# Kernel optimization log

Hardware: AMD Instinct MI355X
Metric: run time of the kernel (lower is better)

## Reference

```python
import jax, jax.numpy as jnp
import numpy as np

N, E, H, EF, NG = 50000, 600000, 128, 4, 20
R_MIN, R_MAX = 0.0, 10.0

def setup_inputs() -> dict:
    key = jax.random.key(0)
    ks = jax.random.split(key, 20)
    s = lambda fi, fo: 1.0 / np.sqrt(fi)
    inp = {
        'h': jax.random.normal(ks[0], (N, H), jnp.float32),
        'x': jax.random.normal(ks[1], (N, 3), jnp.float32),
        'edge_index': jax.random.randint(ks[2], (2, E), 0, N, jnp.int32),
        'mask_ligand': jnp.ones((N,), jnp.float32),
        'edge_attr': jax.random.normal(ks[3], (E, EF), jnp.float32),
        # edge_mlp: Linear(2H+EF+NG,H) silu Linear(H,H) silu
        'We1': jax.random.normal(ks[4], (2*H+EF+NG, H), jnp.float32) * s(2*H+EF+NG, H),
        'be1': jnp.zeros((H,), jnp.float32),
        'We2': jax.random.normal(ks[5], (H, H), jnp.float32) * s(H, H),
        'be2': jnp.zeros((H,), jnp.float32),
        # edge_inf: Linear(H,1) sigmoid
        'Winf': jax.random.normal(ks[6], (H, 1), jnp.float32) * s(H, 1),
        'binf': jnp.zeros((1,), jnp.float32),
        # x_mlp: Linear(H,H) silu Linear(H,1,no bias, gain 0.001) tanh
        'Wx1': jax.random.normal(ks[7], (H, H), jnp.float32) * s(H, H),
        'bx1': jnp.zeros((H,), jnp.float32),
        'Wx2': jax.random.normal(ks[8], (H, 1), jnp.float32) * (0.001 * s(H, 1)),
        # node_mlp: Linear(2H,H) silu Linear(H,H)
        'Wn1': jax.random.normal(ks[9], (2*H, H), jnp.float32) * s(2*H, H),
        'bn1': jnp.zeros((H,), jnp.float32),
        'Wn2': jax.random.normal(ks[10], (H, H), jnp.float32) * s(H, H),
        'bn2': jnp.zeros((H,), jnp.float32),
    }
    return inp

def _gaussian_smearing(d):
    # d: [E,1] -> [E,NG]
    offset = jnp.linspace(R_MIN, R_MAX, NG, dtype=d.dtype)
    coeff = -0.5 / (offset[1] - offset[0]) ** 2
    return jnp.exp(coeff * (d - offset) ** 2)

def reference(h, x, edge_index, mask_ligand, edge_attr,
              We1, be1, We2, be2, Winf, binf, Wx1, bx1, Wx2,
              Wn1, bn1, Wn2, bn2):
    src, dst = edge_index[0], edge_index[1]
    hi, hj = h[dst], h[src]                      # [E,H]
    rel_x = x[dst] - x[src]                      # [E,3]
    d_sq = jnp.sum(rel_x ** 2, -1, keepdims=True)  # [E,1]
    d = jnp.sqrt(d_sq + 1e-8)
    d_feat = _gaussian_smearing(d)               # [E,NG]
    edge_feat = jnp.concatenate([d_feat, edge_attr], -1)
    inp = jnp.concatenate([hi, hj, edge_feat], -1)  # [E,2H+NG+EF]
    mij = jax.nn.silu(jax.nn.silu(inp @ We1 + be1) @ We2 + be2)  # [E,H]
    eij = jax.nn.sigmoid(mij @ Winf + binf)       # [E,1]
    n = h.shape[0]
    mi = jax.ops.segment_sum(mij * eij, dst, num_segments=n)  # [N,H]
    h_new = h + (jax.nn.silu(jnp.concatenate([mi, h], -1) @ Wn1 + bn1) @ Wn2 + bn2)
    gate = jnp.tanh(jax.nn.silu(mij @ Wx1 + bx1) @ Wx2)        # [E,1]
    delta_x = jax.ops.segment_sum(rel_x / (d + 1.0) * gate, dst, num_segments=n)
    x_new = x + delta_x * mask_ligand[:, None]
    return h_new, x_new
```

## Files before the change

### kernel.cpp

```cpp
#include <hip/hip_runtime.h>
#include <hip/hip_bf16.h>
#include <cstdint>

#define NN 50000
#define NE 600000
#define HD 128
#define NG 20
#define EF 4
#define K1 280
#define TILES (NE/64)
#define EGRID 512
#define ROWU 148
#define NTILE 782
#define SW(r) ((r) ^ (((r)>>3)&7))

typedef __attribute__((ext_vector_type(4))) float f32x4;
typedef __attribute__((ext_vector_type(8))) __bf16 bf16x8;
typedef __attribute__((ext_vector_type(4))) unsigned int u32x4;

__device__ __forceinline__ float fast_rcp(float x){ return __builtin_amdgcn_rcpf(x); }
__device__ __forceinline__ float silu_f(float x){ return x * fast_rcp(1.0f + __expf(-x)); }
__device__ __forceinline__ float sigmoid_f(float x){ return fast_rcp(1.0f + __expf(-x)); }
__device__ __forceinline__ float tanh_f(float x){ return 1.0f - 2.0f*fast_rcp(__expf(2.0f*x)+1.0f); }

__device__ __forceinline__ uint32_t pk2(float a, float b){
  uint32_t ua = __float_as_uint(a); ua += 0x7FFFu + ((ua>>16)&1u);
  uint32_t ub = __float_as_uint(b); ub += 0x7FFFu + ((ub>>16)&1u);
  return (ua>>16) | (ub & 0xFFFF0000u);
}
__device__ __forceinline__ uint16_t bfb(float a){
  uint32_t ua = __float_as_uint(a); ua += 0x7FFFu + ((ua>>16)&1u);
  return (uint16_t)(ua>>16);
}
__device__ __forceinline__ float bf2f(uint16_t b){ return __uint_as_float(((uint32_t)b)<<16); }
__device__ __forceinline__ f32x4 MF(u32x4 a, u32x4 b, f32x4 c){
  return __builtin_amdgcn_mfma_f32_16x16x32_bf16(
      __builtin_bit_cast(bf16x8, a), __builtin_bit_cast(bf16x8, b), c, 0, 0, 0);
}

#define EDGE_LDS_U32 (64*ROWU + 4096 + 4096 + 448)
#define EDGE_LDS_B (EDGE_LDS_U32*4)

__global__ void __launch_bounds__(256) h2bf_kernel(
    const float* __restrict__ h, uint32_t* __restrict__ hb)
{
  const size_t i = ((size_t)blockIdx.x*256 + threadIdx.x)*8;
  const float4 a = *reinterpret_cast<const float4*>(h + i);
  const float4 b = *reinterpret_cast<const float4*>(h + i + 4);
  u32x4 v = {pk2(a.x,a.y), pk2(a.z,a.w), pk2(b.x,b.y), pk2(b.z,b.w)};
  *reinterpret_cast<u32x4*>(hb + i/2) = v;
}

template<int BF16H>
__global__ void __launch_bounds__(512, 4) edge_kernel(
    const float* __restrict__ h, const uint32_t* __restrict__ hb,
    const float* __restrict__ x,
    const int* __restrict__ ei, const float* __restrict__ eattr,
    const float* __restrict__ We1, const float* __restrict__ be1,
    const float* __restrict__ We2, const float* __restrict__ be2,
    const float* __restrict__ Winf, const float* __restrict__ binf,
    const float* __restrict__ Wx1, const float* __restrict__ bx1,
    const float* __restrict__ Wx2, float* __restrict__ out)
{
  extern __shared__ uint32_t smem[];
  uint32_t* s_inp = smem;
  uint16_t* t1f   = (uint16_t*)(smem + 64*ROWU);
  uint16_t* mf_   = (uint16_t*)(smem + 64*ROWU + 4096);
  uint32_t* tl    = smem + 64*ROWU + 8192;
  int*   s_dst  = (int*)tl;
  float* s_rel  = (float*)(tl+64);
  float* s_dist = (float*)(tl+256);
  float* s_pe   = (float*)(tl+320);
  float* s_pg   = (float*)(tl+384);

  const int tid = threadIdx.x;
  const int w = tid >> 6, l = tid & 63;
  const int lo = l & 15, hi = l >> 4;
  const int col = w*16 + lo;
  const int r8 = tid >> 3, p8 = tid & 7;
  const int ks2 = w >> 1;
  const int lp  = ((w&1)*2 + (lo>>3))*16 + 4*hi;
  const int jj  = lo & 7;
  const int lsw = SW(l);

  u32x4 B1[9], B2[4], B3[4];
  #pragma unroll
  for (int ks = 0; ks < 9; ++ks){
    float f[8];
    #pragma unroll
    for (int j = 0; j < 8; ++j){
      const int k = ks*32 + hi*8 + j;
      f[j] = (k < K1) ? We1[k*HD + col] : 0.0f;
    }
    B1[ks] = {pk2(f[0],f[1]), pk2(f[2],f[3]), pk2(f[4],f[5]), pk2(f[6],f[7])};
  }
  #pragma unroll
  for (int ks = 0; ks < 4; ++ks){
    float f2[8], f3[8];
    #pragma unroll
    for (int j = 0; j < 8; ++j){
      const int k = ks*32 + hi*8 + j;
      f2[j] = We2[k*HD + col];
      f3[j] = Wx1[k*HD + col];
    }
    B2[ks] = {pk2(f2[0],f2[1]), pk2(f2[2],f2[3]), pk2(f2[4],f2[5]), pk2(f2[6],f2[7])};
    B3[ks] = {pk2(f3[0],f3[1]), pk2(f3[2],f3[3]), pk2(f3[4],f3[5]), pk2(f3[6],f3[7])};
  }
  const float vbe1 = be1[col], vbe2 = be2[col], vbx1 = bx1[col];
  const float wi = Winf[col], wx = Wx2[col], vbinf = binf[0];
  const float SP = 10.0f/19.0f;
  const float CO = -0.5f/(SP*SP);

  int pnode, psj = 0, pdj = 0;
  {
    const int ebase = blockIdx.x*64;
    pnode = (p8 < 4) ? ei[NE + ebase + r8] : ei[ebase + r8];
    if (tid < 64){ psj = ei[ebase + tid]; pdj = ei[NE + ebase + tid]; }
  }

  for (int t = blockIdx.x; t < TILES; t += EGRID){
    const int ebase = t*64;
    __syncthreads();

    if (tid < 64){
      const float ax = x[pdj*3+0]-x[psj*3+0];
      const float ay = x[pdj*3+1]-x[psj*3+1];
      const float az = x[pdj*3+2]-x[psj*3+2];
      const float dd = sqrtf(ax*ax + ay*ay + az*az + 1e-8f);
      s_dst[tid] = pdj;
      s_rel[3*tid+0]=ax; s_rel[3*tid+1]=ay; s_rel[3*tid+2]=az;
      s_dist[tid]=dd; s_pe[tid]=0.0f; s_pg[tid]=0.0f;
      float g[24];
      #pragma unroll
      for (int j = 0; j < 20; ++j){ const float a = dd - j*SP; g[j] = __expf(CO*a*a); }
      const float4 e4 = *reinterpret_cast<const float4*>(eattr + (size_t)(ebase+tid)*EF);
      g[20]=e4.x; g[21]=e4.y; g[22]=e4.z; g[23]=e4.w;
      uint32_t* gp = s_inp + tid*ROWU + 128;
      u32x4 g0v = {pk2(g[0],g[1]),  pk2(g[2],g[3]),  pk2(g[4],g[5]),  pk2(g[6],g[7])};
      u32x4 g1v = {pk2(g[8],g[9]),  pk2(g[10],g[11]),pk2(g[12],g[13]),pk2(g[14],g[15])};
      u32x4 g2v = {pk2(g[16],g[17]),pk2(g[18],g[19]),pk2(g[20],g[21]),pk2(g[22],g[23])};
      u32x4 g3v = {0,0,0,0};
      *reinterpret_cast<u32x4*>(gp)    = g0v;
      *reinterpret_cast<u32x4*>(gp+4)  = g1v;
      *reinterpret_cast<u32x4*>(gp+8)  = g2v;
      *reinterpret_cast<u32x4*>(gp+12) = g3v;
    }
    if (BF16H){
      const uint32_t* hw = hb + (size_t)pnode*(HD/2) + (p8&3)*16;
      uint32_t* dp = s_inp + r8*ROWU + p8*16;
      #pragma unroll
      for (int q = 0; q < 4; ++q)
        *reinterpret_cast<u32x4*>(dp + 4*q) = *reinterpret_cast<const u32x4*>(hw + 4*q);
    } else {
      const float* hp = h + (size_t)pnode*HD + (p8&3)*32;
      uint32_t* dp = s_inp + r8*ROWU + p8*16;
      #pragma unroll
      for (int q = 0; q < 4; ++q){
        const float4 va = *reinterpret_cast<const float4*>(hp + 8*q);
        const float4 vb = *reinterpret_cast<const float4*>(hp + 8*q + 4);
        u32x4 v = { pk2(va.x,va.y), pk2(va.z,va.w), pk2(vb.x,vb.y), pk2(vb.z,vb.w) };
        *reinterpret_cast<u32x4*>(dp + 4*q) = v;
      }
    }
    int np = pnode, ns = psj, nd = pdj;
    if (t + EGRID < TILES){
      const int nb = (t + EGRID)*64;
      np = (p8 < 4) ? ei[NE + nb + r8] : ei[nb + r8];
      if (tid < 64){ ns = ei[nb + tid]; nd = ei[NE + nb + tid]; }
    }
    __syncthreads();

    #pragma unroll
    for (int Mt = 0; Mt < 4; ++Mt){
      const uint32_t* arow = s_inp + (Mt*16 + lo)*ROWU + hi*4;
      f32x4 acc = {0,0,0,0};
      #pragma unroll
      for (int ks = 0; ks < 9; ++ks)
        acc = MF(*reinterpret_cast<const u32x4*>(arow + ks*16), B1[ks], acc);
      #pragma unroll
      for (int reg = 0; reg < 4; ++reg)
        t1f[((Mt*4 + ks2)*64 + SW(lp+reg))*8 + jj] = bfb(silu_f(acc[reg] + vbe1));
    }
    __syncthreads();

    #pragma unroll
    for (int Mt = 0; Mt < 4; ++Mt){
      f32x4 acc = {0,0,0,0};
      #pragma unroll
      for (int ks = 0; ks < 4; ++ks)
        acc = MF(*reinterpret_cast<const u32x4*>(t1f + ((Mt*4+ks)*64 + lsw)*8), B2[ks], acc);
      float p[4];
      #pragma unroll
      for (int reg = 0; reg < 4; ++reg){
        const float m = silu_f(acc[reg] + vbe2);
        mf_[((Mt*4 + ks2)*64 + SW(lp+reg))*8 + jj] = bfb(m);
        p[reg] = m * wi;
      }
      #pragma unroll
      for (int msk = 1; msk < 16; msk <<= 1){
        #pragma unroll
        for (int reg = 0; reg < 4; ++reg) p[reg] += __shfl_xor(p[reg], msk);
      }
      if (lo == 0){
        #pragma unroll
        for (int reg = 0; reg < 4; ++reg) atomicAdd(&s_pe[Mt*16 + 4*hi + reg], p[reg]);
      }
    }
    __syncthreads();

    #pragma unroll
    for (int Mt = 0; Mt < 4; ++Mt){
      #pragma unroll
      for (int reg = 0; reg < 4; ++reg){
        const int r = Mt*16 + 4*hi + reg;
        const float eij = sigmoid_f(s_pe[r] + vbinf);
        const float m = bf2f(mf_[((Mt*4 + ks2)*64 + SW(lp+reg))*8 + jj]);
        atomicAdd(out + (size_t)s_dst[r]*HD + col, m*eij);
      }
    }
    #pragma unroll
    for (int Mt = 0; Mt < 4; ++Mt){
      f32x4 acc = {0,0,0,0};
      #pragma unroll
      for (int ks = 0; ks < 4; ++ks)
        acc = MF(*reinterpret_cast<const u32x4*>(mf_ + ((Mt*4+ks)*64 + lsw)*8), B3[ks], acc);
      float p[4];
      #pragma unroll
      for (int reg = 0; reg < 4; ++reg)
        p[reg] = silu_f(acc[reg] + vbx1) * wx;
      #pragma unroll
      for (int msk = 1; msk < 16; msk <<= 1){
        #pragma unroll
        for (int reg = 0; reg < 4; ++reg) p[reg] += __shfl_xor(p[reg], msk);
      }
      if (lo == 0){
        #pragma unroll
        for (int reg = 0; reg < 4; ++reg) atomicAdd(&s_pg[Mt*16 + 4*hi + reg], p[reg]);
      }
    }
    __syncthreads();

    if (tid < 192){
      const int er = tid/3, c = tid - 3*er;
      const float gate = tanh_f(s_pg[er]);
      const float sc = gate * fast_rcp(s_dist[er] + 1.0f);
      atomicAdd(out + (size_t)NN*HD + (size_t)s_dst[er]*3 + c, s_rel[3*er+c]*sc);
    }

    pnode = np; psj = ns; pdj = nd;
  }
}

#define CROW 132

__global__ void __launch_bounds__(512, 4) node_kernel(
    const float* __restrict__ h, const float* __restrict__ x,
    const float* __restrict__ mask,
    const float* __restrict__ Wn1, const float* __restrict__ bn1,
    const float* __restrict__ Wn2, const float* __restrict__ bn2,
    float* __restrict__ out)
{
  __shared__ uint32_t s_cat[64*CROW];
  __shared__ __align__(16) uint16_t t1n[4*4*64*8];

  const int tid = threadIdx.x;
  const int w = tid >> 6, l = tid & 63;
  const int lo = l & 15, hi = l >> 4;
  const int col = w*16 + lo;

  u32x4 Bn1[8], Bn2[4];
  #pragma unroll
  for (int ks = 0; ks < 8; ++ks){
    float f[8];
    #pragma unroll
    for (int j = 0; j < 8; ++j) f[j] = Wn1[(ks*32 + hi*8 + j)*HD + col];
    Bn1[ks] = {pk2(f[0],f[1]), pk2(f[2],f[3]), pk2(f[4],f[5]), pk2(f[6],f[7])};
  }
  #pragma unroll
  for (int ks = 0; ks < 4; ++ks){
    float f[8];
    #pragma unroll
    for (int j = 0; j < 8; ++j) f[j] = Wn2[(ks*32 + hi*8 + j)*HD + col];
    Bn2[ks] = {pk2(f[0],f[1]), pk2(f[2],f[3]), pk2(f[4],f[5]), pk2(f[6],f[7])};
  }
  const float vbn1 = bn1[col], vbn2 = bn2[col];
  const int nbase = blockIdx.x*64;
  const int ks2 = w >> 1;
  const int lp  = ((w&1)*2 + (lo>>3))*16 + 4*hi;
  const int jj  = lo & 7;

  {
    const int r = tid >> 3, p = tid & 7;
    const int n = nbase + r;
    uint32_t* dp = s_cat + r*CROW + p*16;
    if (n < NN){
      const float* sp = (p < 4) ? (out + (size_t)n*HD + p*32)
                                : (h   + (size_t)n*HD + (p-4)*32);
      #pragma unroll
      for (int q = 0; q < 8; ++q){
        const float4 v = *reinterpret_cast<const float4*>(sp + 4*q);
        dp[2*q]   = pk2(v.x, v.y);
        dp[2*q+1] = pk2(v.z, v.w);
      }
    } else {
      #pragma unroll
      for (int q = 0; q < 16; ++q) dp[q] = 0u;
    }
  }
  __syncthreads();

  #pragma unroll
  for (int Mt = 0; Mt < 4; ++Mt){
    const uint32_t* arow = s_cat + (Mt*16 + lo)*CROW + hi*4;
    f32x4 acc = {0,0,0,0};
    #pragma unroll
    for (int ks = 0; ks < 8; ++ks)
      acc = MF(*reinterpret_cast<const u32x4*>(arow + ks*16), Bn1[ks], acc);
    uint16_t* tp = t1n + ((Mt*4 + ks2)*64 + lp)*8 + jj;
    #pragma unroll
    for (int reg = 0; reg < 4; ++reg)
      tp[reg*8] = bfb(silu_f(acc[reg] + vbn1));
  }
  __syncthreads();

  #pragma unroll
  for (int Mt = 0; Mt < 4; ++Mt){
    f32x4 acc = {0,0,0,0};
    #pragma unroll
    for (int ks = 0; ks < 4; ++ks)
      acc = MF(*reinterpret_cast<const u32x4*>(t1n + ((Mt*4+ks)*64 + l)*8), Bn2[ks], acc);
    #pragma unroll
    for (int reg = 0; reg < 4; ++reg){
      const int n = nbase + Mt*16 + 4*hi + reg;
      if (n < NN)
        out[(size_t)n*HD + col] = h[(size_t)n*HD + col] + acc[reg] + vbn2;
    }
  }

  if (tid < 192){
    const int r = tid/3, c = tid - 3*r;
    const int n = nbase + r;
    if (n < NN){
      const size_t ix = (size_t)NN*HD + (size_t)n*3 + c;
      out[ix] = x[(size_t)n*3 + c] + out[ix]*mask[n];
    }
  }
}

extern "C" void kernel_launch(void* const* d_in, const int* in_sizes, int n_in,
                              void* d_out, int out_size, void* d_ws, size_t ws_size,
                              hipStream_t stream) {
  (void)in_sizes; (void)n_in;
  const float* h    = (const float*)d_in[0];
  const float* x    = (const float*)d_in[1];
  const int*   ei   = (const int*)  d_in[2];
  const float* mask = (const float*)d_in[3];
  const float* ea   = (const float*)d_in[4];
  const float* We1  = (const float*)d_in[5];
  const float* be1  = (const float*)d_in[6];
  const float* We2  = (const float*)d_in[7];
  const float* be2  = (const float*)d_in[8];
  const float* Winf = (const float*)d_in[9];
  const float* binf = (const float*)d_in[10];
  const float* Wx1  = (const float*)d_in[11];
  const float* bx1  = (const float*)d_in[12];
  const float* Wx2  = (const float*)d_in[13];
  const float* Wn1  = (const float*)d_in[14];
  const float* bn1  = (const float*)d_in[15];
  const float* Wn2  = (const float*)d_in[16];
  const float* bn2  = (const float*)d_in[17];
  float* out = (float*)d_out;

  const bool use_bf = ws_size >= (size_t)NN*HD*2;
  uint32_t* hb = (uint32_t*)d_ws;

  hipFuncSetAttribute(reinterpret_cast<const void*>(edge_kernel<1>),
                      hipFuncAttributeMaxDynamicSharedMemorySize, EDGE_LDS_B);
  hipFuncSetAttribute(reinterpret_cast<const void*>(edge_kernel<0>),
                      hipFuncAttributeMaxDynamicSharedMemorySize, EDGE_LDS_B);

  hipMemsetAsync(d_out, 0, (size_t)out_size * sizeof(float), stream);

  if (use_bf){
    h2bf_kernel<<<3125, 256, 0, stream>>>(h, hb);
    edge_kernel<1><<<EGRID, 512, EDGE_LDS_B, stream>>>(
        h, hb, x, ei, ea, We1, be1, We2, be2, Winf, binf, Wx1, bx1, Wx2, out);
  } else {
    edge_kernel<0><<<EGRID, 512, EDGE_LDS_B, stream>>>(
        h, hb, x, ei, ea, We1, be1, We2, be2, Winf, binf, Wx1, bx1, Wx2, out);
  }
  node_kernel<<<NTILE, 512, 0, stream>>>(
      h, x, mask, Wn1, bn1, Wn2, bn2, out);
}
```

Measured before the change: 459.3 us.

## Sort edges by destination via counting sort and pre-reduce scatter in LDS

Adds a histogram, scan and fill pass that builds a destination-sorted permutation of the edges. The edge kernel then processes edges in that order, accumulates messages per unique destination in shared memory, and issues one global atomic per unique destination row instead of one per edge. This is meant to cut global atomic traffic and contention for both the message and the coordinate sums. In exchange it adds several small kernels plus an atomic-based fill, an indirect gather through perm, and loses the previous index prefetch. Because the fill uses atomics, edge order within a destination is not deterministic.

Result: slower. 889.1 us (+93.6%).

```diff
diff --git a/kernel.cpp b/kernel.cpp
--- a/kernel.cpp
+++ b/kernel.cpp
@@ -38,9 +38,6 @@
       __builtin_bit_cast(bf16x8, a), __builtin_bit_cast(bf16x8, b), c, 0, 0, 0);
 }
 
-#define EDGE_LDS_U32 (64*ROWU + 4096 + 4096 + 448)
-#define EDGE_LDS_B (EDGE_LDS_U32*4)
-
 __global__ void __launch_bounds__(256) h2bf_kernel(
     const float* __restrict__ h, uint32_t* __restrict__ hb)
 {
@@ -51,10 +48,271 @@
   *reinterpret_cast<u32x4*>(hb + i/2) = v;
 }
 
-template<int BF16H>
-__global__ void __launch_bounds__(512, 4) edge_kernel(
-    const float* __restrict__ h, const uint32_t* __restrict__ hb,
-    const float* __restrict__ x,
+__global__ void __launch_bounds__(512) hist_kernel(
+    const int* __restrict__ ei, int* __restrict__ cnt)
+{
+  const int e = blockIdx.x*512 + threadIdx.x;
+  if (e < NE) atomicAdd(&cnt[ei[NE + e]], 1);
+}
+
+__global__ void __launch_bounds__(512) scanA_kernel(
+    int* __restrict__ cur, int* __restrict__ bsums)
+{
+  __shared__ int s[512];
+  const int tid = threadIdx.x;
+  const int i = blockIdx.x*512 + tid;
+  const int v = (i < NN) ? cur[i] : 0;
+  s[tid] = v; __syncthreads();
+  #pragma unroll
+  for (int d = 1; d < 512; d <<= 1){
+    const int t = (tid >= d) ? s[tid-d] : 0;
+    __syncthreads();
+    s[tid] += t;
+    __syncthreads();
+  }
+  if (i < NN) cur[i] = s[tid] - v;
+  if (tid == 511) bsums[blockIdx.x] = s[511];
+}
+
+__global__ void scanB_kernel(int* __restrict__ bsums)
+{
+  if (threadIdx.x == 0 && blockIdx.x == 0){
+    int acc = 0;
+    for (int b = 0; b < 98; ++b){ const int t = bsums[b]; bsums[b] = acc; acc += t; }
+  }
+}
+
+__global__ void __launch_bounds__(512) scanC_kernel(
+    int* __restrict__ cur, const int* __restrict__ bsums)
+{
+  const int i = blockIdx.x*512 + threadIdx.x;
+  if (i < NN) cur[i] += bsums[blockIdx.x];
+}
+
+__global__ void __launch_bounds__(512) fill_kernel(
+    const int* __restrict__ ei, int* __restrict__ cur, int* __restrict__ perm)
+{
+  const int e = blockIdx.x*512 + threadIdx.x;
+  if (e < NE){
+    const int p = atomicAdd(&cur[ei[NE + e]], 1);
+    perm[p] = e;
+  }
+}
+
+#define EDGE_LDS_U32 (64*ROWU + 4096 + 4096 + 784)
+#define EDGE_LDS_B (EDGE_LDS_U32*4)
+
+__global__ void __launch_bounds__(512, 4) edge_csr_kernel(
+    const uint32_t* __restrict__ hb, const float* __restrict__ x,
+    const int* __restrict__ ei, const float* __restrict__ eattr,
+    const int* __restrict__ perm,
+    const float* __restrict__ We1, const float* __restrict__ be1,
+    const float* __restrict__ We2, const float* __restrict__ be2,
+    const float* __restrict__ Winf, const float* __restrict__ binf,
+    const float* __restrict__ Wx1, const float* __restrict__ bx1,
+    const float* __restrict__ Wx2, float* __restrict__ out)
+{
+  extern __shared__ uint32_t smem[];
+  uint32_t* s_inp = smem;
+  float*    uacc  = (float*)smem;
+  uint16_t* t1f   = (uint16_t*)(smem + 64*ROWU);
+  uint16_t* mf_   = (uint16_t*)(smem + 64*ROWU + 4096);
+  uint32_t* tl    = smem + 64*ROWU + 8192;
+  int*   s_dst  = (int*)tl;
+  float* s_rel  = (float*)(tl+64);
+  float* s_dist = (float*)(tl+256);
+  float* s_pe   = (float*)(tl+320);
+  float* s_pg   = (float*)(tl+384);
+  int*   s_slot = (int*)(tl+448);
+  int*   s_udst = (int*)(tl+512);
+  float* s_uax  = (float*)(tl+576);
+  int*   s_Un   = (int*)(tl+768);
+
+  const int tid = threadIdx.x;
+  const int w = tid >> 6, l = tid & 63;
+  const int lo = l & 15, hi = l >> 4;
+  const int col = w*16 + lo;
+  const int r8 = tid >> 3, p8 = tid & 7;
+  const int ks2 = w >> 1;
+  const int lp  = ((w&1)*2 + (lo>>3))*16 + 4*hi;
+  const int jj  = lo & 7;
+  const int lsw = SW(l);
+
+  u32x4 B1[9], B2[4], B3[4];
+  #pragma unroll
+  for (int ks = 0; ks < 9; ++ks){
+    float f[8];
+    #pragma unroll
+    for (int j = 0; j < 8; ++j){
+      const int k = ks*32 + hi*8 + j;
+      f[j] = (k < K1) ? We1[k*HD + col] : 0.0f;
+    }
+    B1[ks] = {pk2(f[0],f[1]), pk2(f[2],f[3]), pk2(f[4],f[5]), pk2(f[6],f[7])};
+  }
+  #pragma unroll
+  for (int ks = 0; ks < 4; ++ks){
+    float f2[8], f3[8];
+    #pragma unroll
+    for (int j = 0; j < 8; ++j){
+      const int k = ks*32 + hi*8 + j;
+      f2[j] = We2[k*HD + col];
+      f3[j] = Wx1[k*HD + col];
+    }
+    B2[ks] = {pk2(f2[0],f2[1]), pk2(f2[2],f2[3]), pk2(f2[4],f2[5]), pk2(f2[6],f2[7])};
+    B3[ks] = {pk2(f3[0],f3[1]), pk2(f3[2],f3[3]), pk2(f3[4],f3[5]), pk2(f3[6],f3[7])};
+  }
+  const float vbe1 = be1[col], vbe2 = be2[col], vbx1 = bx1[col];
+  const float wi = Winf[col], wx = Wx2[col], vbinf = binf[0];
+  const float SP = 10.0f/19.0f;
+  const float CO = -0.5f/(SP*SP);
+
+  for (int t = blockIdx.x; t < TILES; t += EGRID){
+    const int ebase = t*64;
+    __syncthreads();
+
+    if (tid < 64){
+      const int e = perm[ebase + tid];
+      const int sj = ei[e], dj = ei[NE + e];
+      const float ax = x[dj*3+0]-x[sj*3+0];
+      const float ay = x[dj*3+1]-x[sj*3+1];
+      const float az = x[dj*3+2]-x[sj*3+2];
+      const float dd = sqrtf(ax*ax + ay*ay + az*az + 1e-8f);
+      s_dst[tid] = dj;
+      s_rel[3*tid+0]=ax; s_rel[3*tid+1]=ay; s_rel[3*tid+2]=az;
+      s_dist[tid]=dd; s_pe[tid]=0.0f; s_pg[tid]=0.0f;
+      const int dprev = __shfl_up(dj, 1);
+      const int isnew = (tid == 0) || (dj != dprev);
+      const unsigned long long m = __ballot(isnew);
+      const int slot = __popcll(m << (63 - tid)) - 1;
+      s_slot[tid] = slot;
+      if (isnew) s_udst[slot] = dj;
+      if (tid == 63) s_Un[0] = slot + 1;
+      s_uax[3*tid+0]=0.0f; s_uax[3*tid+1]=0.0f; s_uax[3*tid+2]=0.0f;
+      float g[24];
+      #pragma unroll
+      for (int j = 0; j < 20; ++j){ const float a = dd - j*SP; g[j] = __expf(CO*a*a); }
+      const float4 e4 = *reinterpret_cast<const float4*>(eattr + (size_t)e*EF);
+      g[20]=e4.x; g[21]=e4.y; g[22]=e4.z; g[23]=e4.w;
+      uint32_t* gp = s_inp + tid*ROWU + 128;
+      u32x4 g0v = {pk2(g[0],g[1]),  pk2(g[2],g[3]),  pk2(g[4],g[5]),  pk2(g[6],g[7])};
+      u32x4 g1v = {pk2(g[8],g[9]),  pk2(g[10],g[11]),pk2(g[12],g[13]),pk2(g[14],g[15])};
+      u32x4 g2v = {pk2(g[16],g[17]),pk2(g[18],g[19]),pk2(g[20],g[21]),pk2(g[22],g[23])};
+      u32x4 g3v = {0,0,0,0};
+      *reinterpret_cast<u32x4*>(gp)    = g0v;
+      *reinterpret_cast<u32x4*>(gp+4)  = g1v;
+      *reinterpret_cast<u32x4*>(gp+8)  = g2v;
+      *reinterpret_cast<u32x4*>(gp+12) = g3v;
+    }
+    {
+      const int e = perm[ebase + r8];
+      const int node = (p8 < 4) ? ei[NE + e] : ei[e];
+      const uint32_t* hw = hb + (size_t)node*(HD/2) + (p8&3)*16;
+      uint32_t* dp = s_inp + r8*ROWU + p8*16;
+      #pragma unroll
+      for (int q = 0; q < 4; ++q)
+        *reinterpret_cast<u32x4*>(dp + 4*q) = *reinterpret_cast<const u32x4*>(hw + 4*q);
+    }
+    __syncthreads();
+
+    #pragma unroll
+    for (int Mt = 0; Mt < 4; ++Mt){
+      const uint32_t* arow = s_inp + (Mt*16 + lo)*ROWU + hi*4;
+      f32x4 acc = {0,0,0,0};
+      #pragma unroll
+      for (int ks = 0; ks < 9; ++ks)
+        acc = MF(*reinterpret_cast<const u32x4*>(arow + ks*16), B1[ks], acc);
+      #pragma unroll
+      for (int reg = 0; reg < 4; ++reg)
+        t1f[((Mt*4 + ks2)*64 + SW(lp+reg))*8 + jj] = bfb(silu_f(acc[reg] + vbe1));
+    }
+    __syncthreads();
+
+    const int U = s_Un[0];
+    for (int idx = tid; idx < U*32; idx += 512)
+      *reinterpret_cast<u32x4*>((uint32_t*)uacc + idx*4) = u32x4{0,0,0,0};
+
+    #pragma unroll
+    for (int Mt = 0; Mt < 4; ++Mt){
+      f32x4 acc = {0,0,0,0};
+      #pragma unroll
+      for (int ks = 0; ks < 4; ++ks)
+        acc = MF(*reinterpret_cast<const u32x4*>(t1f + ((Mt*4+ks)*64 + lsw)*8), B2[ks], acc);
+      float p[4];
+      #pragma unroll
+      for (int reg = 0; reg < 4; ++reg){
+        const float m = silu_f(acc[reg] + vbe2);
+        mf_[((Mt*4 + ks2)*64 + SW(lp+reg))*8 + jj] = bfb(m);
+        p[reg] = m * wi;
+      }
+      #pragma unroll
+      for (int msk = 1; msk < 16; msk <<= 1){
+        #pragma unroll
+        for (int reg = 0; reg < 4; ++reg) p[reg] += __shfl_xor(p[reg], msk);
+      }
+      if (lo == 0){
+        #pragma unroll
+        for (int reg = 0; reg < 4; ++reg) atomicAdd(&s_pe[Mt*16 + 4*hi + reg], p[reg]);
+      }
+    }
+    __syncthreads();
+
+    #pragma unroll
+    for (int Mt = 0; Mt < 4; ++Mt){
+      #pragma unroll
+      for (int reg = 0; reg < 4; ++reg){
+        const int r = Mt*16 + 4*hi + reg;
+        const float eij = sigmoid_f(s_pe[r] + vbinf);
+        const float m = bf2f(mf_[((Mt*4 + ks2)*64 + SW(lp+reg))*8 + jj]);
+        atomicAdd(&uacc[s_slot[r]*HD + col], m*eij);
+      }
+    }
+    #pragma unroll
+    for (int Mt = 0; Mt < 4; ++Mt){
+      f32x4 acc = {0,0,0,0};
+      #pragma unroll
+      for (int ks = 0; ks < 4; ++ks)
+        acc = MF(*reinterpret_cast<const u32x4*>(mf_ + ((Mt*4+ks)*64 + lsw)*8), B3[ks], acc);
+      float p[4];
+      #pragma unroll
+      for (int reg = 0; reg < 4; ++reg)
+        p[reg] = silu_f(acc[reg] + vbx1) * wx;
+      #pragma unroll
+      for (int msk = 1; msk < 16; msk <<= 1){
+        #pragma unroll
+        for (int reg = 0; reg < 4; ++reg) p[reg] += __shfl_xor(p[reg], msk);
+      }
+      if (lo == 0){
+        #pragma unroll
+        for (int reg = 0; reg < 4; ++reg) atomicAdd(&s_pg[Mt*16 + 4*hi + reg], p[reg]);
+      }
+    }
+    __syncthreads();
+
+    if (tid < 192){
+      const int er = tid/3, c = tid - 3*er;
+      const float gate = tanh_f(s_pg[er]);
+      const float sc = gate * fast_rcp(s_dist[er] + 1.0f);
+      atomicAdd(&s_uax[s_slot[er]*3 + c], s_rel[3*er+c]*sc);
+    }
+    __syncthreads();
+
+    {
+      const int c = tid & 127;
+      for (int u = tid >> 7; u < U; u += 4)
+        atomicAdd(out + (size_t)s_udst[u]*HD + c, uacc[u*HD + c]);
+      for (int q = tid; q < U*3; q += 512){
+        const int u = q/3, cc = q - 3*u;
+        atomicAdd(out + (size_t)NN*HD + (size_t)s_udst[u]*3 + cc, s_uax[q]);
+      }
+    }
+  }
+}
+
+#define FB_LDS_U32 (64*ROWU + 4096 + 4096 + 448)
+#define FB_LDS_B (FB_LDS_U32*4)
+
+__global__ void __launch_bounds__(512, 4) edge_fb_kernel(
+    const float* __restrict__ h, const float* __restrict__ x,
     const int* __restrict__ ei, const float* __restrict__ eattr,
     const float* __restrict__ We1, const float* __restrict__ be1,
     const float* __restrict__ We2, const float* __restrict__ be2,
@@ -111,23 +369,16 @@
   const float SP = 10.0f/19.0f;
   const float CO = -0.5f/(SP*SP);
 
-  int pnode, psj = 0, pdj = 0;
-  {
-    const int ebase = blockIdx.x*64;
-    pnode = (p8 < 4) ? ei[NE + ebase + r8] : ei[ebase + r8];
-    if (tid < 64){ psj = ei[ebase + tid]; pdj = ei[NE + ebase + tid]; }
-  }
-
   for (int t = blockIdx.x; t < TILES; t += EGRID){
     const int ebase = t*64;
     __syncthreads();
-
     if (tid < 64){
-      const float ax = x[pdj*3+0]-x[psj*3+0];
-      const float ay = x[pdj*3+1]-x[psj*3+1];
-      const float az = x[pdj*3+2]-x[psj*3+2];
+      const int sj = ei[ebase+tid], dj = ei[NE+ebase+tid];
+      const float ax = x[dj*3+0]-x[sj*3+0];
+      const float ay = x[dj*3+1]-x[sj*3+1];
+      const float az = x[dj*3+2]-x[sj*3+2];
       const float dd = sqrtf(ax*ax + ay*ay + az*az + 1e-8f);
-      s_dst[tid] = pdj;
+      s_dst[tid] = dj;
       s_rel[3*tid+0]=ax; s_rel[3*tid+1]=ay; s_rel[3*tid+2]=az;
       s_dist[tid]=dd; s_pe[tid]=0.0f; s_pg[tid]=0.0f;
       float g[24];
@@ -145,14 +396,10 @@
       *reinterpret_cast<u32x4*>(gp+8)  = g2v;
       *reinterpret_cast<u32x4*>(gp+12) = g3v;
     }
-    if (BF16H){
-      const uint32_t* hw = hb + (size_t)pnode*(HD/2) + (p8&3)*16;
-      uint32_t* dp = s_inp + r8*ROWU + p8*16;
-      #pragma unroll
-      for (int q = 0; q < 4; ++q)
-        *reinterpret_cast<u32x4*>(dp + 4*q) = *reinterpret_cast<const u32x4*>(hw + 4*q);
-    } else {
-      const float* hp = h + (size_t)pnode*HD + (p8&3)*32;
+    {
+      const int e = ebase + r8;
+      const int node = (p8 < 4) ? ei[NE + e] : ei[e];
+      const float* hp = h + (size_t)node*HD + (p8&3)*32;
       uint32_t* dp = s_inp + r8*ROWU + p8*16;
       #pragma unroll
       for (int q = 0; q < 4; ++q){
@@ -162,12 +409,6 @@
         *reinterpret_cast<u32x4*>(dp + 4*q) = v;
       }
     }
-    int np = pnode, ns = psj, nd = pdj;
-    if (t + EGRID < TILES){
-      const int nb = (t + EGRID)*64;
-      np = (p8 < 4) ? ei[NE + nb + r8] : ei[nb + r8];
-      if (tid < 64){ ns = ei[nb + tid]; nd = ei[NE + nb + tid]; }
-    }
     __syncthreads();
 
     #pragma unroll
@@ -246,8 +487,6 @@
       const float sc = gate * fast_rcp(s_dist[er] + 1.0f);
       atomicAdd(out + (size_t)NN*HD + (size_t)s_dst[er]*3 + c, s_rel[3*er+c]*sc);
     }
-
-    pnode = np; psj = ns; pdj = nd;
   }
 }
 
@@ -371,23 +610,33 @@
   const float* bn2  = (const float*)d_in[17];
   float* out = (float*)d_out;
 
-  const bool use_bf = ws_size >= (size_t)NN*HD*2;
-  uint32_t* hb = (uint32_t*)d_ws;
-
-  hipFuncSetAttribute(reinterpret_cast<const void*>(edge_kernel<1>),
+  uint32_t* hb   = (uint32_t*)d_ws;
+  int* cursor    = (int*)d_ws + 3200000;
+  int* perm      = (int*)d_ws + 3250000;
+  int* bsums     = (int*)d_ws + 3850000;
+  const size_t need = (size_t)(3850000 + 128) * 4;
+  const bool use_csr = ws_size >= need;
+
+  hipFuncSetAttribute(reinterpret_cast<const void*>(edge_csr_kernel),
                       hipFuncAttributeMaxDynamicSharedMemorySize, EDGE_LDS_B);
-  hipFuncSetAttribute(reinterpret_cast<const void*>(edge_kernel<0>),
-                      hipFuncAttributeMaxDynamicSharedMemorySize, EDGE_LDS_B);
+  hipFuncSetAttribute(reinterpret_cast<const void*>(edge_fb_kernel),
+                      hipFuncAttributeMaxDynamicSharedMemorySize, FB_LDS_B);
 
   hipMemsetAsync(d_out, 0, (size_t)out_size * sizeof(float), stream);
 
-  if (use_bf){
+  if (use_csr){
+    hipMemsetAsync(cursor, 0, (size_t)NN*4, stream);
     h2bf_kernel<<<3125, 256, 0, stream>>>(h, hb);
-    edge_kernel<1><<<EGRID, 512, EDGE_LDS_B, stream>>>(
-        h, hb, x, ei, ea, We1, be1, We2, be2, Winf, binf, Wx1, bx1, Wx2, out);
+    hist_kernel<<<1172, 512, 0, stream>>>(ei, cursor);
+    scanA_kernel<<<98, 512, 0, stream>>>(cursor, bsums);
+    scanB_kernel<<<1, 64, 0, stream>>>(bsums);
+    scanC_kernel<<<98, 512, 0, stream>>>(cursor, bsums);
+    fill_kernel<<<1172, 512, 0, stream>>>(ei, cursor, perm);
+    edge_csr_kernel<<<EGRID, 512, EDGE_LDS_B, stream>>>(
+        hb, x, ei, ea, perm, We1, be1, We2, be2, Winf, binf, Wx1, bx1, Wx2, out);
   } else {
-    edge_kernel<0><<<EGRID, 512, EDGE_LDS_B, stream>>>(
-        h, hb, x, ei, ea, We1, be1, We2, be2, Winf, binf, Wx1, bx1, Wx2, out);
+    edge_fb_kernel<<<EGRID, 512, FB_LDS_B, stream>>>(
+        h, x, ei, ea, We1, be1, We2, be2, Winf, binf, Wx1, bx1, Wx2, out);
   }
   node_kernel<<<NTILE, 512, 0, stream>>>(
       h, x, mask, Wn1, bn1, Wn2, bn2, out);
```
